# Performance work log

Hardware: AMD Instinct MI355X
Metric: run time of the kernel (lower is better)

Reference implementation:

```python
import jax, jax.numpy as jnp
import numpy as np

B, S, D_MODEL = 2, 2048, 4096
N_HEADS, N_KV, HEAD_DIM = 32, 8, 128
N_GROUPS = N_HEADS // N_KV
QKV_DIM = (N_HEADS + 2 * N_KV) * HEAD_DIM


def _rope_tables(seq_len, head_dim, base=10000.0):
    inv_freq = 1.0 / (base ** (np.arange(0, head_dim, 2, dtype=np.float32) / head_dim))
    t = np.arange(seq_len, dtype=np.float32)
    freqs = np.outer(t, inv_freq)                      # [S, D/2]
    emb = np.concatenate([freqs, freqs], axis=-1)      # [S, D]
    return jnp.asarray(np.cos(emb)), jnp.asarray(np.sin(emb))


def setup_inputs() -> dict:
    key = jax.random.key(0)
    k1, k2, k3 = jax.random.split(key, 3)
    cos, sin = _rope_tables(S, HEAD_DIM)
    return {
        "hidden_states": jax.random.normal(k1, (B, S, D_MODEL), dtype=jnp.float32),
        "cos": cos,
        "sin": sin,
        "W_qkv": jax.random.normal(k2, (D_MODEL, QKV_DIM), dtype=jnp.float32) * (D_MODEL ** -0.5),
        "W_out": jax.random.normal(k3, (D_MODEL, D_MODEL), dtype=jnp.float32) * (D_MODEL ** -0.5),
    }


def _rotate_half(x):
    x1, x2 = jnp.split(x, 2, axis=-1)
    return jnp.concatenate([-x2, x1], axis=-1)


def _apply_rope(x, cos, sin):
    # x: [b, h, s, d]; cos/sin: [s, d]
    c = cos[None, None, :, :]
    s = sin[None, None, :, :]
    return x * c + _rotate_half(x) * s


def reference(hidden_states, cos, sin, W_qkv, W_out):
    b, s, _ = hidden_states.shape
    qkv = jnp.einsum("bsm,mq->bsq", hidden_states, W_qkv)
    q_end = N_HEADS * HEAD_DIM
    kv_sz = N_KV * HEAD_DIM
    q = qkv[..., :q_end].reshape(b, s, N_HEADS, HEAD_DIM).transpose(0, 2, 1, 3)
    k = qkv[..., q_end:q_end + kv_sz].reshape(b, s, N_KV, HEAD_DIM).transpose(0, 2, 1, 3)
    v = qkv[..., q_end + kv_sz:].reshape(b, s, N_KV, HEAD_DIM).transpose(0, 2, 1, 3)

    q = _apply_rope(q, cos, sin)          # [b, H, s, d]
    k = _apply_rope(k, cos, sin)          # [b, KV, s, d] (equiv. to repeat->rope->stride slice)

    # GQA without materializing repeated KV: group query heads per KV head.
    qg = q.reshape(b, N_KV, N_GROUPS, s, HEAD_DIM)
    scale = HEAD_DIM ** -0.5
    scores = jnp.einsum("bkgqd,bkpd->bkgqp", qg, k) * scale  # [b, KV, G, s, s]
    causal = jnp.tril(jnp.ones((s, s), dtype=bool))
    scores = jnp.where(causal, scores, jnp.finfo(scores.dtype).min)
    probs = jax.nn.softmax(scores, axis=-1)
    out = jnp.einsum("bkgqp,bkpd->bkgqd", probs, v)           # [b, KV, G, s, d]
    out = out.reshape(b, N_HEADS, s, HEAD_DIM).transpose(0, 2, 1, 3).reshape(b, s, D_MODEL)
    return jnp.einsum("bsm,mn->bsn", out, W_out)
```

## Files before the change

kernel.cpp:

```cpp
#include <hip/hip_runtime.h>


typedef __bf16 bf16;
typedef bf16 bf16x8 __attribute__((ext_vector_type(8)));
typedef bf16 bf16x4 __attribute__((ext_vector_type(4)));
typedef float f32x4 __attribute__((ext_vector_type(4)));
typedef unsigned int u32;
typedef u32 u32x4 __attribute__((ext_vector_type(4)));

#define B_ 2
#define S_ 2048
#define DM 4096
#define NH 32
#define NKV 8
#define HD 128
#define QKV_DIM 6144

typedef __attribute__((address_space(3))) void lds_void;
typedef const __attribute__((address_space(1))) void glb_void;

__device__ __forceinline__ void gld_lds16(const bf16* g, bf16* l) {
  __builtin_amdgcn_global_load_lds((glb_void*)g, (lds_void*)l, 16, 0, 0);
}

__device__ __forceinline__ u32 bf16bits(float x) {
  union { bf16 h; unsigned short s; } u;
  u.h = (bf16)x;
  return (u32)u.s;
}

#define BAR() __builtin_amdgcn_s_barrier()
#define VM4() asm volatile("s_waitcnt vmcnt(4)" ::: "memory")
#define VM0() asm volatile("s_waitcnt vmcnt(0)" ::: "memory")
#define PRIO1() __builtin_amdgcn_s_setprio(1)
#define PRIO0() __builtin_amdgcn_s_setprio(0)

__global__ __launch_bounds__(256) void cast_f32_bf16(const float* __restrict__ src,
                                                     bf16* __restrict__ dst, int n) {
  int i = (blockIdx.x * 256 + threadIdx.x) * 4;
  float4 v = *(const float4*)(src + i);
  bf16x4 o;
  o[0] = (bf16)v.x; o[1] = (bf16)v.y; o[2] = (bf16)v.z; o[3] = (bf16)v.w;
  *(bf16x4*)(dst + i) = o;
}

__global__ __launch_bounds__(256) void transpose_cast_w(const float* __restrict__ W,
                                                        bf16* __restrict__ Wt,
                                                        int K, int N) {
  __shared__ float tile[64][65];
  const int n0 = blockIdx.x * 64, k0 = blockIdx.y * 64;
  const int t = threadIdx.x, j = t & 63, i0 = t >> 6;
  for (int p = 0; p < 16; ++p) {
    int i = i0 + p * 4;
    tile[i][j] = W[(size_t)(k0 + i) * N + n0 + j];
  }
  __syncthreads();
  for (int p = 0; p < 16; ++p) {
    int n = i0 + p * 4;
    Wt[(size_t)(n0 + n) * K + k0 + j] = (bf16)tile[j][n];
  }
}

__global__ __launch_bounds__(256) void transpose_v(const bf16* __restrict__ qkv,
                                                   bf16* __restrict__ v_t) {
  __shared__ bf16 tile[64][65];
  const int s0 = blockIdx.x * 64;
  const int d0 = blockIdx.y * 64;
  const int bk = blockIdx.z;
  const int b = bk >> 3, kv = bk & 7;
  const int t = threadIdx.x, j = t & 63, i0 = t >> 6;
  const bf16* src = qkv + (size_t)b * S_ * QKV_DIM + 5120 + kv * HD;
  for (int p = 0; p < 16; ++p) {
    int i = i0 + p * 4;
    tile[i][j] = src[(size_t)(s0 + i) * QKV_DIM + d0 + j];
  }
  __syncthreads();
  bf16* dst = v_t + ((size_t)bk * HD + d0) * S_ + s0;
  for (int p = 0; p < 16; ++p) {
    int dd = i0 + p * 4;
    dst[(size_t)dd * S_ + j] = tile[j][dd];
  }
}

__global__ __launch_bounds__(320) void rope_kernel(const bf16* __restrict__ qkv,
                                                   const float* __restrict__ cosT,
                                                   const float* __restrict__ sinT,
                                                   bf16* __restrict__ q_r,
                                                   bf16* __restrict__ k_r) {
  const int bs = blockIdx.x;
  const int b = bs >> 11, s = bs & 2047;
  const int t = threadIdx.x;
  const int hh = t >> 3;
  const int g = (t & 7) * 8;
  const bool isQ = hh < NH;
  const bf16* row = qkv + (size_t)bs * QKV_DIM + (isQ ? hh * HD : DM + (hh - NH) * HD);
  bf16x8 xl8 = *(const bf16x8*)(row + g);
  bf16x8 xh8 = *(const bf16x8*)(row + g + 64);
  const float* cbase = cosT + (size_t)s * HD;
  const float* sbase = sinT + (size_t)s * HD;
  float cl[8], sl[8], ch[8], sh[8];
  *(float4*)(cl) = *(const float4*)(cbase + g);
  *(float4*)(cl + 4) = *(const float4*)(cbase + g + 4);
  *(float4*)(ch) = *(const float4*)(cbase + g + 64);
  *(float4*)(ch + 4) = *(const float4*)(cbase + g + 68);
  *(float4*)(sl) = *(const float4*)(sbase + g);
  *(float4*)(sl + 4) = *(const float4*)(sbase + g + 4);
  *(float4*)(sh) = *(const float4*)(sbase + g + 64);
  *(float4*)(sh + 4) = *(const float4*)(sbase + g + 68);
  const float scale = isQ ? 0.08838834764831845f : 1.0f;
  bf16x8 ol8, oh8;
#pragma unroll
  for (int j = 0; j < 8; ++j) {
    const float xl = (float)xl8[j], xh = (float)xh8[j];
    ol8[j] = (bf16)((xl * cl[j] - xh * sl[j]) * scale);
    oh8[j] = (bf16)((xh * ch[j] + xl * sh[j]) * scale);
  }
  bf16* dst = isQ ? (q_r + (((size_t)(b * NH + hh)) * S_ + s) * HD)
                  : (k_r + (((size_t)(b * NKV + (hh - NH))) * S_ + s) * HD);
  *(bf16x8*)(dst + g) = ol8;
  *(bf16x8*)(dst + g + 64) = oh8;
}

template <bool OUT_BF16, int BM, int BN>
__global__ __launch_bounds__(512, 2) void gemm_bt(const bf16* __restrict__ A,
                                                  const bf16* __restrict__ Bt,
                                                  void* __restrict__ Cout,
                                                  int M, int N, int K) {
  constexpr int MF = BM / 32;
  constexpr int NF = BN / 64;
  constexpr int NCA = BM / 128;
  constexpr int NCB = BN / 128;
  constexpr int AKH = BM * 64;
  constexpr int BKH = BN * 64;
  constexpr int BUF = 2 * (AKH + BKH);
  extern __shared__ char lds[];
  const int NT = K >> 6;

  const int nwg = gridDim.x;
  const int cpx = nwg >> 3;
  const int wg = (blockIdx.x & 7) * cpx + (blockIdx.x >> 3);
  const int nbx = N / BN;
  const int bx = wg % nbx, by = wg / nbx;
  const int m0 = by * BM, n0 = bx * BN;

  const int t = threadIdx.x;
  const int w = t >> 6, lane = t & 63;
  const int wr = w >> 2, wc = w & 3;
  const int quad = lane >> 4, c = lane & 15;

  const int aOff = (((wr * (BM / 2) + c) * 64 + quad * 16) ^ ((c & 8) << 2));
  const int bOff = 2 * AKH + ((((wc * (BN / 4) + c) * 64 + quad * 16) ^ ((c & 8) << 2)));

  const int scol = (((lane & 3) ^ ((lane >> 4) & 2)) << 3);
  const bf16* gA[NCA];
  const bf16* gB[NCB];
#pragma unroll
  for (int cc = 0; cc < NCA; ++cc)
    gA[cc] = A + (size_t)(m0 + w * (BM / 8) + cc * 16 + (lane >> 2)) * K + scol;
#pragma unroll
  for (int cc = 0; cc < NCB; ++cc)
    gB[cc] = Bt + (size_t)(n0 + w * (BN / 8) + cc * 16 + (lane >> 2)) * K + scol;

  auto stageKh = [&](int P, int kh, int ke) {
    char* ab = lds + P * BUF + kh * AKH + w * (BM * 8);
#pragma unroll
    for (int cc = 0; cc < NCA; ++cc) gld_lds16(gA[cc] + ke, (bf16*)(ab + cc * 1024));
    char* bb = lds + P * BUF + 2 * AKH + kh * BKH + w * (BN * 8);
#pragma unroll
    for (int cc = 0; cc < NCB; ++cc) gld_lds16(gB[cc] + ke, (bf16*)(bb + cc * 1024));
  };

  bf16x8 a0[MF], b0v[NF], a1[MF], b1v[NF];
  auto ldFr = [&](int P, int kh, bf16x8* av, bf16x8* bv) {
    const char* ab = lds + P * BUF + kh * AKH + aOff;
#pragma unroll
    for (int i = 0; i < MF; ++i) av[i] = *(const bf16x8*)(ab + i * 1024);
    const char* bb = lds + P * BUF + kh * BKH + bOff;
#pragma unroll
    for (int j = 0; j < NF; ++j) bv[j] = *(const bf16x8*)(bb + j * 1024);
  };

  f32x4 acc[MF][NF];
#pragma unroll
  for (int i = 0; i < MF; ++i)
#pragma unroll
    for (int j = 0; j < NF; ++j) acc[i][j] = (f32x4){0.f, 0.f, 0.f, 0.f};

  auto mfmac = [&](bf16x8* av, bf16x8* bv) {
    PRIO1();
#pragma unroll
    for (int i = 0; i < MF; ++i)
#pragma unroll
      for (int j = 0; j < NF; ++j)
        acc[i][j] = __builtin_amdgcn_mfma_f32_16x16x32_bf16(av[i], bv[j], acc[i][j], 0, 0, 0);
    PRIO0();
  };

  auto gtile = [&](int P, bool S0, bool S1) {
    BAR();
    ldFr(P, 0, a0, b0v);
    if (S0) stageKh(P ^ 1, 1, 96);
    mfmac(a0, b0v);
    ldFr(P, 1, a1, b1v);
    BAR();
    if (S1) stageKh(P, 0, 128);
    mfmac(a1, b1v);
  };

  auto adv = [&]() {
#pragma unroll
    for (int cc = 0; cc < NCA; ++cc) gA[cc] += 64;
#pragma unroll
    for (int cc = 0; cc < NCB; ++cc) gB[cc] += 64;
  };

  stageKh(0, 0, 0); stageKh(0, 1, 32); stageKh(1, 0, 64);
  VM4();

  for (int tt = 0; tt < NT - 2; tt += 2) {
    gtile(0, true, true); VM4(); adv();
    gtile(1, true, true); VM4(); adv();
  }
  gtile(0, true, false); VM0();
  gtile(1, false, false);

  const int crow = m0 + wr * (BM / 2) + quad * 4;
  const int ccol = n0 + wc * (BN / 4) + c;
#pragma unroll
  for (int mf = 0; mf < MF; ++mf)
#pragma unroll
    for (int nn = 0; nn < NF; ++nn) {
      const int row = crow + mf * 16;
      const int col = ccol + nn * 16;
      if constexpr (OUT_BF16) {
        bf16* Cp = (bf16*)Cout;
#pragma unroll
        for (int r = 0; r < 4; ++r) Cp[(size_t)(row + r) * N + col] = (bf16)acc[mf][nn][r];
      } else {
        float* Cp = (float*)Cout;
#pragma unroll
        for (int r = 0; r < 4; ++r) Cp[(size_t)(row + r) * N + col] = acc[mf][nn][r];
      }
    }
}

#define QBLK 64
#define KVB 64
__global__ __launch_bounds__(256, 2) void attn_kernel(const bf16* __restrict__ q_r,
                                                      const bf16* __restrict__ k_r,
                                                      const bf16* __restrict__ v_t,
                                                      bf16* __restrict__ attn_out) {
  __shared__ bf16 Ks[KVB * HD];
  __shared__ bf16 Vs[HD * KVB];

  const int qb = blockIdx.x, bh = blockIdx.y;
  const int b = bh >> 5, h = bh & 31;
  const int kv = h >> 2;
  const int q0 = qb * QBLK;
  const int t = threadIdx.x, w = t >> 6, lane = t & 63;
  const int quad = lane >> 4, c = lane & 15;
  const int myq = q0 + w * 16 + c;

  const bf16* qrow = q_r + ((size_t)(b * NH + h) * S_ + myq) * HD;
  bf16x8 qf[4];
#pragma unroll
  for (int kk = 0; kk < 4; ++kk) qf[kk] = *(const bf16x8*)(qrow + quad * 8 + kk * 32);

  float m_i = -1e30f, l_i = 0.f;
  f32x4 o_acc[8];
#pragma unroll
  for (int n = 0; n < 8; ++n) o_acc[n] = (f32x4){0.f, 0.f, 0.f, 0.f};

  const bf16* kb_ptr = k_r + (size_t)(b * NKV + kv) * S_ * HD;
  const bf16* vb_ptr = v_t + (size_t)(b * NKV + kv) * HD * S_;
  const int nch = qb + 1;

  const int lr = lane >> 4, lc = lane & 15;
  const int kcol0 = (((lc << 4) ^ (lr << 4)) >> 1);
  const int kcol1 = (((lc << 4) ^ ((lr + 4) << 4)) >> 1);
  const int vlr = lane >> 3, vlc = lane & 7;
  const int vcol = (((vlc << 4) ^ (vlr << 4)) >> 1);
  const int fxor = (c & 7) << 3;

  const int src0 = c + 32 * (quad & 1);
  const int src1 = src0 + 16;
  const bool hiTile = (quad & 2) != 0;

  auto packP = [&](const float* ea, const float* eb) -> bf16x8 {
    u32 pk[4];
#pragma unroll
    for (int r = 0; r < 4; ++r) pk[r] = bf16bits(ea[r]) | (bf16bits(eb[r]) << 16);
    u32 a0[4], a1[4];
#pragma unroll
    for (int r = 0; r < 4; ++r) {
      a0[r] = (u32)__shfl((int)pk[r], src0, 64);
      a1[r] = (u32)__shfl((int)pk[r], src1, 64);
    }
    u32 w0, w1, w2, w3;
    if (hiTile) {
      w0 = (a0[0] >> 16) | (a0[1] & 0xffff0000u);
      w1 = (a0[2] >> 16) | (a0[3] & 0xffff0000u);
      w2 = (a1[0] >> 16) | (a1[1] & 0xffff0000u);
      w3 = (a1[2] >> 16) | (a1[3] & 0xffff0000u);
    } else {
      w0 = (a0[0] & 0xffffu) | (a0[1] << 16);
      w1 = (a0[2] & 0xffffu) | (a0[3] << 16);
      w2 = (a1[0] & 0xffffu) | (a1[1] << 16);
      w3 = (a1[2] & 0xffffu) | (a1[3] << 16);
    }
    return __builtin_bit_cast(bf16x8, (u32x4){w0, w1, w2, w3});
  };

  for (int ch = 0; ch < nch; ++ch) {
    const int kb = ch * KVB;
#pragma unroll
    for (int j = 0; j < 4; ++j) {
      const bf16* gk = kb_ptr + (size_t)(kb + w * 16 + j * 4 + lr) * HD +
                       ((j & 1) ? kcol1 : kcol0);
      gld_lds16(gk, Ks + (w * 16 + j * 4) * HD);
      const bf16* gv = vb_ptr + (size_t)(w * 32 + j * 8 + vlr) * S_ + kb + vcol;
      gld_lds16(gv, Vs + (w * 32 + j * 8) * KVB);
    }
    VM0();
    BAR();

    const int wmax = q0 + w * 16 + 15;
    if (kb <= wmax) {
      const bool hi = (kb + 32 <= wmax);
      f32x4 st0 = (f32x4){0.f, 0.f, 0.f, 0.f};
      f32x4 st1 = (f32x4){0.f, 0.f, 0.f, 0.f};
      f32x4 st2 = (f32x4){0.f, 0.f, 0.f, 0.f};
      f32x4 st3 = (f32x4){0.f, 0.f, 0.f, 0.f};
#pragma unroll
      for (int kk = 0; kk < 4; ++kk) {
        const int kx = (quad * 8 + kk * 32) ^ fxor;
        bf16x8 kf0 = *(const bf16x8*)(Ks + (c)*HD + kx);
        bf16x8 kf1 = *(const bf16x8*)(Ks + (16 + c) * HD + kx);
        st0 = __builtin_amdgcn_mfma_f32_16x16x32_bf16(kf0, qf[kk], st0, 0, 0, 0);
        st1 = __builtin_amdgcn_mfma_f32_16x16x32_bf16(kf1, qf[kk], st1, 0, 0, 0);
      }
      if (hi) {
#pragma unroll
        for (int kk = 0; kk < 4; ++kk) {
          const int kx = (quad * 8 + kk * 32) ^ fxor;
          bf16x8 kf2 = *(const bf16x8*)(Ks + (32 + c) * HD + kx);
          bf16x8 kf3 = *(const bf16x8*)(Ks + (48 + c) * HD + kx);
          st2 = __builtin_amdgcn_mfma_f32_16x16x32_bf16(kf2, qf[kk], st2, 0, 0, 0);
          st3 = __builtin_amdgcn_mfma_f32_16x16x32_bf16(kf3, qf[kk], st3, 0, 0, 0);
        }
      }

      float e0[4], e1[4], e2[4], e3[4];
#pragma unroll
      for (int r = 0; r < 4; ++r) { e0[r] = st0[r]; e1[r] = st1[r]; e2[r] = st2[r]; e3[r] = st3[r]; }
      const int key0 = kb + quad * 4;
      if (kb + 31 > q0 + w * 16) {
#pragma unroll
        for (int r = 0; r < 4; ++r) {
          if (key0 + r > myq) e0[r] = -1e30f;
          if (key0 + 16 + r > myq) e1[r] = -1e30f;
        }
      }
      if (hi && kb + 63 > q0 + w * 16) {
#pragma unroll
        for (int r = 0; r < 4; ++r) {
          if (key0 + 32 + r > myq) e2[r] = -1e30f;
          if (key0 + 48 + r > myq) e3[r] = -1e30f;
        }
      }

      float mloc = fmaxf(fmaxf(fmaxf(e0[0], e0[1]), fmaxf(e0[2], e0[3])),
                         fmaxf(fmaxf(e1[0], e1[1]), fmaxf(e1[2], e1[3])));
      if (hi)
        mloc = fmaxf(mloc, fmaxf(fmaxf(fmaxf(e2[0], e2[1]), fmaxf(e2[2], e2[3])),
                                 fmaxf(fmaxf(e3[0], e3[1]), fmaxf(e3[2], e3[3]))));
      mloc = fmaxf(mloc, __shfl_xor(mloc, 16, 64));
      mloc = fmaxf(mloc, __shfl_xor(mloc, 32, 64));
      const bool defer = (__all(mloc - m_i <= 8.0f) != 0);
      const float mnew = defer ? m_i : fmaxf(m_i, mloc);
      float sum = 0.f;
#pragma unroll
      for (int r = 0; r < 4; ++r) {
        e0[r] = __expf(e0[r] - mnew); sum += e0[r];
        e1[r] = __expf(e1[r] - mnew); sum += e1[r];
      }
      if (hi) {
#pragma unroll
        for (int r = 0; r < 4; ++r) {
          e2[r] = __expf(e2[r] - mnew); sum += e2[r];
          e3[r] = __expf(e3[r] - mnew); sum += e3[r];
        }
      }
      sum += __shfl_xor(sum, 16, 64);
      sum += __shfl_xor(sum, 32, 64);
      if (!defer) {
        const float alpha = __expf(m_i - mnew);
        m_i = mnew;
        l_i = l_i * alpha + sum;
        float alpha_o[4];
#pragma unroll
        for (int r = 0; r < 4; ++r) alpha_o[r] = __shfl(alpha, quad * 4 + r, 64);
#pragma unroll
        for (int n = 0; n < 8; ++n)
#pragma unroll
          for (int r = 0; r < 4; ++r) o_acc[n][r] *= alpha_o[r];
      } else {
        l_i += sum;
      }

      bf16x8 pf0 = packP(e0, e1);
#pragma unroll
      for (int n = 0; n < 8; ++n) {
        bf16x8 vf0 = *(const bf16x8*)(Vs + (n * 16 + c) * KVB + ((quad * 8) ^ fxor));
        o_acc[n] = __builtin_amdgcn_mfma_f32_16x16x32_bf16(pf0, vf0, o_acc[n], 0, 0, 0);
      }
      if (hi) {
        bf16x8 pf1 = packP(e2, e3);
#pragma unroll
        for (int n = 0; n < 8; ++n) {
          bf16x8 vf1 = *(const bf16x8*)(Vs + (n * 16 + c) * KVB + ((quad * 8 + 32) ^ fxor));
          o_acc[n] = __builtin_amdgcn_mfma_f32_16x16x32_bf16(pf1, vf1, o_acc[n], 0, 0, 0);
        }
      }
    }
    BAR();
  }

  float l_o[4];
#pragma unroll
  for (int r = 0; r < 4; ++r) l_o[r] = __shfl(l_i, quad * 4 + r, 64);
#pragma unroll
  for (int n = 0; n < 8; ++n)
#pragma unroll
    for (int r = 0; r < 4; ++r) {
      const int row = q0 + w * 16 + quad * 4 + r;
      const float ov = o_acc[n][r] / l_o[r];
      attn_out[((size_t)b * S_ + row) * DM + h * HD + n * 16 + c] = (bf16)ov;
    }
}

extern "C" void kernel_launch(void* const* d_in, const int* in_sizes, int n_in,
                              void* d_out, int out_size, void* d_ws, size_t ws_size,
                              hipStream_t stream) {
  const float* hidden = (const float*)d_in[0];
  const float* cosT = (const float*)d_in[1];
  const float* sinT = (const float*)d_in[2];
  const float* Wqkv = (const float*)d_in[3];
  const float* Wout = (const float*)d_in[4];
  float* out = (float*)d_out;
  char* ws = (char*)d_ws;

  bf16* WqkvT = (bf16*)(ws + 0);
  bf16* q_r = (bf16*)(ws + 0);
  bf16* k_r = (bf16*)(ws + 33554432);
  bf16* WoutT = (bf16*)(ws + 50331648);
  bf16* h_bf = (bf16*)(ws + 83886080);
  bf16* attn_out = (bf16*)(ws + 83886080);
  bf16* v_t = (bf16*)(ws + 117440512);
  bf16* qkv = (bf16*)d_out;

  static bool attr_set = false;
  if (!attr_set) {
    hipFuncSetAttribute(reinterpret_cast<const void*>(&gemm_bt<true, 128, 384>),
                        hipFuncAttributeMaxDynamicSharedMemorySize, 131072);
    hipFuncSetAttribute(reinterpret_cast<const void*>(&gemm_bt<false, 256, 256>),
                        hipFuncAttributeMaxDynamicSharedMemorySize, 131072);
    attr_set = true;
  }

  cast_f32_bf16<<<dim3(16384), dim3(256), 0, stream>>>(hidden, h_bf, B_ * S_ * DM);
  transpose_cast_w<<<dim3(QKV_DIM / 64, DM / 64), dim3(256), 0, stream>>>(Wqkv, WqkvT, DM, QKV_DIM);
  transpose_cast_w<<<dim3(DM / 64, DM / 64), dim3(256), 0, stream>>>(Wout, WoutT, DM, DM);
  gemm_bt<true, 128, 384><<<dim3((QKV_DIM / 384) * ((B_ * S_) / 128)), dim3(512), 131072, stream>>>(
      h_bf, WqkvT, (void*)qkv, B_ * S_, QKV_DIM, DM);
  rope_kernel<<<dim3(B_ * S_), dim3(320), 0, stream>>>(qkv, cosT, sinT, q_r, k_r);
  transpose_v<<<dim3(S_ / 64, HD / 64, B_ * NKV), dim3(256), 0, stream>>>(qkv, v_t);
  attn_kernel<<<dim3(S_ / QBLK, B_ * NH), dim3(256), 0, stream>>>(q_r, k_r, v_t, attn_out);
  gemm_bt<false, 256, 256><<<dim3((DM / 256) * ((B_ * S_) / 256)), dim3(512), 131072, stream>>>(
      attn_out, WoutT, (void*)out, B_ * S_, DM, DM);
}
```

Measured before the change: 819.2 us.

## Double-buffer K/V tiles in attention, reverse block order, raise MFMA priority

The attention kernel now keeps two LDS buffers for K and V. It issues the async global-to-LDS load of the next KV chunk before computing on the current one, so load latency overlaps with the MFMA work. Query blocks are launched in reverse order so the longest causal blocks start first and the tail is more balanced. s_setprio is raised around the MFMA sections. LDS usage doubles per block, which could limit occupancy.

After: 873.5 us. +6.6%, slower.

```diff
diff --git a/kernel.cpp b/kernel.cpp
--- a/kernel.cpp
+++ b/kernel.cpp
@@ -250,10 +250,11 @@
                                                       const bf16* __restrict__ k_r,
                                                       const bf16* __restrict__ v_t,
                                                       bf16* __restrict__ attn_out) {
-  __shared__ bf16 Ks[KVB * HD];
-  __shared__ bf16 Vs[HD * KVB];
-
-  const int qb = blockIdx.x, bh = blockIdx.y;
+  __shared__ bf16 Ks[2][KVB * HD];
+  __shared__ bf16 Vs[2][HD * KVB];
+
+  const int qb = gridDim.x - 1 - blockIdx.x;
+  const int bh = blockIdx.y;
   const int b = bh >> 5, h = bh & 31;
   const int kv = h >> 2;
   const int q0 = qb * QBLK;
@@ -281,6 +282,17 @@
   const int vlr = lane >> 3, vlc = lane & 7;
   const int vcol = (((vlc << 4) ^ (vlr << 4)) >> 1);
   const int fxor = (c & 7) << 3;
+
+  auto stage = [&](int P, int kb) {
+#pragma unroll
+    for (int j = 0; j < 4; ++j) {
+      const bf16* gk = kb_ptr + (size_t)(kb + w * 16 + j * 4 + lr) * HD +
+                       ((j & 1) ? kcol1 : kcol0);
+      gld_lds16(gk, Ks[P] + (w * 16 + j * 4) * HD);
+      const bf16* gv = vb_ptr + (size_t)(w * 32 + j * 8 + vlr) * S_ + kb + vcol;
+      gld_lds16(gv, Vs[P] + (w * 32 + j * 8) * KVB);
+    }
+  };
 
   const int src0 = c + 32 * (quad & 1);
   const int src1 = src0 + 16;
@@ -311,18 +323,14 @@
     return __builtin_bit_cast(bf16x8, (u32x4){w0, w1, w2, w3});
   };
 
+  stage(0, 0);
+  VM0();
+  BAR();
+
   for (int ch = 0; ch < nch; ++ch) {
     const int kb = ch * KVB;
-#pragma unroll
-    for (int j = 0; j < 4; ++j) {
-      const bf16* gk = kb_ptr + (size_t)(kb + w * 16 + j * 4 + lr) * HD +
-                       ((j & 1) ? kcol1 : kcol0);
-      gld_lds16(gk, Ks + (w * 16 + j * 4) * HD);
-      const bf16* gv = vb_ptr + (size_t)(w * 32 + j * 8 + vlr) * S_ + kb + vcol;
-      gld_lds16(gv, Vs + (w * 32 + j * 8) * KVB);
-    }
-    VM0();
-    BAR();
+    const int P = ch & 1;
+    if (ch + 1 < nch) stage(P ^ 1, kb + KVB);
 
     const int wmax = q0 + w * 16 + 15;
     if (kb <= wmax) {
@@ -331,11 +339,12 @@
       f32x4 st1 = (f32x4){0.f, 0.f, 0.f, 0.f};
       f32x4 st2 = (f32x4){0.f, 0.f, 0.f, 0.f};
       f32x4 st3 = (f32x4){0.f, 0.f, 0.f, 0.f};
+      PRIO1();
 #pragma unroll
       for (int kk = 0; kk < 4; ++kk) {
         const int kx = (quad * 8 + kk * 32) ^ fxor;
-        bf16x8 kf0 = *(const bf16x8*)(Ks + (c)*HD + kx);
-        bf16x8 kf1 = *(const bf16x8*)(Ks + (16 + c) * HD + kx);
+        bf16x8 kf0 = *(const bf16x8*)(Ks[P] + (c)*HD + kx);
+        bf16x8 kf1 = *(const bf16x8*)(Ks[P] + (16 + c) * HD + kx);
         st0 = __builtin_amdgcn_mfma_f32_16x16x32_bf16(kf0, qf[kk], st0, 0, 0, 0);
         st1 = __builtin_amdgcn_mfma_f32_16x16x32_bf16(kf1, qf[kk], st1, 0, 0, 0);
       }
@@ -343,12 +352,13 @@
 #pragma unroll
         for (int kk = 0; kk < 4; ++kk) {
           const int kx = (quad * 8 + kk * 32) ^ fxor;
-          bf16x8 kf2 = *(const bf16x8*)(Ks + (32 + c) * HD + kx);
-          bf16x8 kf3 = *(const bf16x8*)(Ks + (48 + c) * HD + kx);
+          bf16x8 kf2 = *(const bf16x8*)(Ks[P] + (32 + c) * HD + kx);
+          bf16x8 kf3 = *(const bf16x8*)(Ks[P] + (48 + c) * HD + kx);
           st2 = __builtin_amdgcn_mfma_f32_16x16x32_bf16(kf2, qf[kk], st2, 0, 0, 0);
           st3 = __builtin_amdgcn_mfma_f32_16x16x32_bf16(kf3, qf[kk], st3, 0, 0, 0);
         }
       }
+      PRIO0();
 
       float e0[4], e1[4], e2[4], e3[4];
 #pragma unroll
@@ -409,20 +419,25 @@
       }
 
       bf16x8 pf0 = packP(e0, e1);
+      PRIO1();
 #pragma unroll
       for (int n = 0; n < 8; ++n) {
-        bf16x8 vf0 = *(const bf16x8*)(Vs + (n * 16 + c) * KVB + ((quad * 8) ^ fxor));
+        bf16x8 vf0 = *(const bf16x8*)(Vs[P] + (n * 16 + c) * KVB + ((quad * 8) ^ fxor));
         o_acc[n] = __builtin_amdgcn_mfma_f32_16x16x32_bf16(pf0, vf0, o_acc[n], 0, 0, 0);
       }
+      PRIO0();
       if (hi) {
         bf16x8 pf1 = packP(e2, e3);
+        PRIO1();
 #pragma unroll
         for (int n = 0; n < 8; ++n) {
-          bf16x8 vf1 = *(const bf16x8*)(Vs + (n * 16 + c) * KVB + ((quad * 8 + 32) ^ fxor));
+          bf16x8 vf1 = *(const bf16x8*)(Vs[P] + (n * 16 + c) * KVB + ((quad * 8 + 32) ^ fxor));
           o_acc[n] = __builtin_amdgcn_mfma_f32_16x16x32_bf16(pf1, vf1, o_acc[n], 0, 0, 0);
         }
-      }
-    }
+        PRIO0();
+      }
+    }
+    VM0();
     BAR();
   }
 
```
